# Performance work log

Hardware: AMD Instinct MI355X
Metric: run time of the kernel (lower is better)

The kernel has to match this reference:

```python
import jax, jax.numpy as jnp
import numpy as np

B, S, H, DK, DM = 8, 2048, 8, 64, 512  # batch, seq, heads, head dim, model dim
NEG = jnp.float32(-2**31)  # fill value for float32 per source


def setup_inputs() -> dict:
    key = jax.random.key(0)
    ks = jax.random.split(key, 8)
    q = jax.random.normal(ks[0], (B, S, DK), dtype=jnp.float32)
    k = jax.random.normal(ks[1], (B, S, DK), dtype=jnp.float32)
    v = jax.random.normal(ks[2], (B, S, DK), dtype=jnp.float32)
    mask = jax.random.randint(ks[3], (B, S, S), 0, 2).astype(jnp.float32)
    # torch Linear params stored as [in, out] for x @ W + b
    Wq = jax.random.normal(ks[4], (DK, H * DK), dtype=jnp.float32) / np.sqrt(DK).astype(np.float32)
    bq = jax.random.normal(ks[5], (H * DK,), dtype=jnp.float32) * 0.02
    Wo = jax.random.normal(ks[6], (H * DK, DM), dtype=jnp.float32) / np.sqrt(H * DK).astype(np.float32)
    bo = jax.random.normal(ks[7], (DM,), dtype=jnp.float32) * 0.02
    return {"q": q, "k": k, "v": v, "mask": mask, "Wq": Wq, "bq": bq, "Wo": Wo, "bo": bo}


def reference(q, k, v, mask, Wq, bq, Wo, bo):
    # Faithful to the source BUG: linear_q projects q, k AND v.
    def proj(x):
        b, s, _ = x.shape
        return (x @ Wq + bq).reshape(b, s, H, DK).transpose(2, 0, 1, 3)  # [H,B,S,DK]

    qh, kh, vh = proj(q), proj(k), proj(v)
    e = jnp.einsum('hbqd,hbkd->hbqk', qh, kh) / np.float32(np.sqrt(DK))  # [H,B,Sq,Sk]
    # source fills where ((mask-1).bool()==False), i.e. where mask == 1.0
    e = jnp.where(mask[None] == 1.0, NEG, e)
    a = jax.nn.softmax(e, axis=-1)
    y = jnp.einsum('hbqk,hbkd->hbqd', a, vh)          # [H,B,Sq,DK]
    y = y.transpose(1, 2, 0, 3).reshape(B, S, H * DK)  # [B,Sq,H*DK]
    return y @ Wo + bo
```

## Files before the change

kernel.cpp:

```cpp
#include <hip/hip_runtime.h>
#include <hip/hip_bf16.h>

#define BB 8
#define SS 2048
#define HD 512
#define DM 512

typedef __attribute__((ext_vector_type(8))) short short8;
typedef __attribute__((ext_vector_type(4))) short short4v;
typedef __attribute__((ext_vector_type(4))) float floatx4;

__device__ __forceinline__ short f2bf(float f) {
    __hip_bfloat16 h = __float2bfloat16(f);
    short s;
    __builtin_memcpy(&s, &h, 2);
    return s;
}

__device__ __forceinline__ uint2 pack4bf(float a, float b, float cc, float d) {
    __hip_bfloat162 lo = __float22bfloat162_rn(float2{a, b});
    __hip_bfloat162 hi = __float22bfloat162_rn(float2{cc, d});
    uint2 r;
    __builtin_memcpy(&r.x, &lo, 4);
    __builtin_memcpy(&r.y, &hi, 4);
    return r;
}

__device__ __forceinline__ short4v pack4bf_s4(float a, float b, float cc, float d) {
    uint2 u = pack4bf(a, b, cc, d);
    short4v s;
    __builtin_memcpy(&s, &u, 8);
    return s;
}

__device__ __forceinline__ floatx4 mfma16(short4v a, short4v b, floatx4 c) {
#if __has_builtin(__builtin_amdgcn_mfma_f32_16x16x16_bf16)
    return __builtin_amdgcn_mfma_f32_16x16x16_bf16(a, b, c, 0, 0, 0);
#else
    return __builtin_amdgcn_mfma_f32_16x16x16bf16_1k(a, b, c, 0, 0, 0);
#endif
}

__global__ void prep_kernel(const float* __restrict__ Wq, const float* __restrict__ Wo,
                            short* __restrict__ WqT, short* __restrict__ WoT) {
    int idx = blockIdx.x * 256 + threadIdx.x;
    if (idx < HD * 64) {
        int o = idx >> 6, i = idx & 63;
        WqT[idx] = f2bf(Wq[i * HD + o]);
    }
    {
        int o = idx >> 9, i = idx & 511;
        WoT[idx] = f2bf(Wo[i * DM + o]);
    }
}

__global__ void maskbits_kernel(const float* __restrict__ mask,
                                unsigned long long* __restrict__ bits) {
    int gw = blockIdx.x * 4 + (threadIdx.x >> 6);
    int lane = threadIdx.x & 63;
    size_t base = (size_t)gw * 256;
    float4 v = *(const float4*)(mask + base + (size_t)lane * 4);
    unsigned long long nib =
        (v.x == 1.0f ? 1ull : 0ull) | (v.y == 1.0f ? 2ull : 0ull) |
        (v.z == 1.0f ? 4ull : 0ull) | (v.w == 1.0f ? 8ull : 0ull);
    unsigned long long word = nib << (4 * (lane & 15));
    word |= __shfl_xor(word, 1);
    word |= __shfl_xor(word, 2);
    word |= __shfl_xor(word, 4);
    word |= __shfl_xor(word, 8);
    if ((lane & 15) == 0) bits[gw * 4 + (lane >> 4)] = word;
}

template <int SMODE, bool BIAS_ROW, bool A_F32, bool B_F32>
__global__ __launch_bounds__(256, 2) void gemm_bt(
    const void* __restrict__ A_, int lda, long sA,
    const void* __restrict__ B_, int ldb, long sB,
    void* __restrict__ C, int ldc, long sC,
    const float* __restrict__ bias, int K, float alpha) {
    const int bz = blockIdx.z;
    const int m0 = blockIdx.y * 128, n0 = blockIdx.x * 128;
    __shared__ __align__(16) short As[128 * 80];
    __shared__ __align__(16) short Bs[128 * 80];
    const int tid = threadIdx.x, lane = tid & 63, w = tid >> 6;
    const int c = lane & 15, Q = lane >> 4;
    const int wm = w >> 1, wn = w & 1;
    floatx4 acc[4][4] = {};

    for (int k0 = 0; k0 < K; k0 += 64) {
#pragma unroll
        for (int it = 0; it < 4; ++it) {
            int chunk = it * 256 + tid;
            int row = chunk >> 3, c8 = chunk & 7;
            size_t aoff = (size_t)bz * sA + (size_t)(m0 + row) * lda + k0 + c8 * 8;
            size_t boff = (size_t)bz * sB + (size_t)(n0 + row) * ldb + k0 + c8 * 8;
            if (A_F32) {
                const float* Af = (const float*)A_ + aoff;
                float4 lo = *(const float4*)Af;
                float4 hi = *(const float4*)(Af + 4);
                uint2 p0 = pack4bf(lo.x, lo.y, lo.z, lo.w);
                uint2 p1 = pack4bf(hi.x, hi.y, hi.z, hi.w);
                *(uint4*)&As[row * 80 + c8 * 8] = uint4{p0.x, p0.y, p1.x, p1.y};
            } else {
                *(uint4*)&As[row * 80 + c8 * 8] = *(const uint4*)((const short*)A_ + aoff);
            }
            if (B_F32) {
                const float* Bf = (const float*)B_ + boff;
                float4 lo = *(const float4*)Bf;
                float4 hi = *(const float4*)(Bf + 4);
                uint2 p0 = pack4bf(lo.x, lo.y, lo.z, lo.w);
                uint2 p1 = pack4bf(hi.x, hi.y, hi.z, hi.w);
                *(uint4*)&Bs[row * 80 + c8 * 8] = uint4{p0.x, p0.y, p1.x, p1.y};
            } else {
                *(uint4*)&Bs[row * 80 + c8 * 8] = *(const uint4*)((const short*)B_ + boff);
            }
        }
        __syncthreads();
#pragma unroll
        for (int ks = 0; ks < 2; ++ks) {
            short8 af[4], bf[4];
#pragma unroll
            for (int mt = 0; mt < 4; ++mt)
                af[mt] = *(const short8*)&As[(wm * 64 + mt * 16 + c) * 80 + ks * 32 + 8 * Q];
#pragma unroll
            for (int nt = 0; nt < 4; ++nt)
                bf[nt] = *(const short8*)&Bs[(wn * 64 + nt * 16 + c) * 80 + ks * 32 + 8 * Q];
#pragma unroll
            for (int mt = 0; mt < 4; ++mt)
#pragma unroll
                for (int nt = 0; nt < 4; ++nt)
                    acc[mt][nt] = __builtin_amdgcn_mfma_f32_16x16x32_bf16(
                        af[mt], bf[nt], acc[mt][nt], 0, 0, 0);
        }
        __syncthreads();
    }
#pragma unroll
    for (int mt = 0; mt < 4; ++mt)
#pragma unroll
        for (int nt = 0; nt < 4; ++nt) {
            int col = n0 + wn * 64 + nt * 16 + c;
            float bc = BIAS_ROW ? 0.f : bias[col];
#pragma unroll
            for (int r = 0; r < 4; ++r) {
                int row = m0 + wm * 64 + mt * 16 + 4 * Q + r;
                float val = (acc[mt][nt][r] + (BIAS_ROW ? bias[row] : bc)) * alpha;
                if (SMODE == 0) {
                    ((float*)C)[(size_t)bz * sC + (size_t)row * ldc + col] = val;
                } else if (SMODE == 1) {
                    ((short*)C)[(size_t)bz * sC + (size_t)row * ldc + col] = f2bf(val);
                } else if (SMODE == 2) {
                    int b = row >> 11, s = row & 2047, h = col >> 6, d = col & 63;
                    size_t idx = ((size_t)(b * 8 + h)) * 131072 + (size_t)s * 64 +
                                 (size_t)(((d >> 3) ^ (s & 7)) * 8 + (d & 7));
                    ((short*)C)[idx] = f2bf(val);
                } else {
                    int h = row >> 6, d = row & 63, s = col;
                    size_t idx = ((size_t)(bz * 8 + h)) * 131072 + (size_t)(s >> 3) * 512 +
                                 (size_t)((d ^ ((s >> 3) & 15)) * 8 + (s & 7));
                    ((short*)C)[idx] = f2bf(val);
                }
            }
        }
}

__global__ __launch_bounds__(512, 2) void fa_kernel(
    const short* __restrict__ qh, const short* __restrict__ khS,
    const short* __restrict__ vI, const unsigned* __restrict__ mbits,
    short* __restrict__ y) {
    const int id = blockIdx.x;
    const int xcd = id & 7, slot = id >> 3;
    const int qt = slot & 7;
    const int bh = (slot >> 3) * 8 + xcd;
    const int b = bh >> 3, h = bh & 7;
    const int tid = threadIdx.x, lane = tid & 63, w = tid >> 6;
    const int c = lane & 15, Q = lane >> 4;
    const int c7 = c & 7;

    __shared__ __align__(16) short Ks[8192];
    __shared__ __align__(16) short Vs[8192];

    const int qbase0 = qt * 256 + w * 32;
    short8 qf[2][2];
#pragma unroll
    for (int t = 0; t < 2; ++t) {
        const short* qb = qh + ((size_t)(b * SS + qbase0 + t * 16 + c)) * HD + h * 64;
        qf[t][0] = *(const short8*)(qb + 8 * Q);
        qf[t][1] = *(const short8*)(qb + 32 + 8 * Q);
    }
    const unsigned* mrow[2] = {
        mbits + (size_t)(b * SS + qbase0 + c) * 64,
        mbits + (size_t)(b * SS + qbase0 + 16 + c) * 64};

    const short* kbase = khS + (size_t)bh * 131072;
    const short* vbase = vI + (size_t)bh * 131072;

    floatx4 o[2][4] = {};
    float m_i[2] = {-INFINITY, -INFINITY}, l_i[2] = {0.f, 0.f};

    for (int kt = 0; kt < 16; ++kt) {
        const short* kg = kbase + kt * 8192;
        const short* vg = vbase + kt * 8192;
#pragma unroll
        for (int it = 0; it < 2; ++it) {
            int off = (it * 512 + tid) * 8;
            *(uint4*)&Ks[off] = *(const uint4*)(kg + off);
            *(uint4*)&Vs[off] = *(const uint4*)(vg + off);
        }
        uint4 mr[2];
#pragma unroll
        for (int t = 0; t < 2; ++t) mr[t] = *(const uint4*)(mrow[t] + kt * 4);
        __syncthreads();

        floatx4 s[2][8];
        float mx[2] = {-INFINITY, -INFINITY};
#pragma unroll
        for (int jt = 0; jt < 8; ++jt) {
            short8 k0 = *(const short8*)&Ks[(16 * jt + c) * 64 + ((Q) ^ c7) * 8];
            short8 k1 = *(const short8*)&Ks[(16 * jt + c) * 64 + ((Q + 4) ^ c7) * 8];
#pragma unroll
            for (int t = 0; t < 2; ++t) {
                floatx4 z = {};
                z = __builtin_amdgcn_mfma_f32_16x16x32_bf16(k0, qf[t][0], z, 0, 0, 0);
                z = __builtin_amdgcn_mfma_f32_16x16x32_bf16(k1, qf[t][1], z, 0, 0, 0);
                unsigned mwd = (jt & 2) ? ((jt & 4) ? mr[t].w : mr[t].y)
                                        : ((jt & 4) ? mr[t].z : mr[t].x);
                unsigned nib = (mwd >> (((jt & 1) << 4) + 4 * Q)) & 0xFu;
#pragma unroll
                for (int r = 0; r < 4; ++r) {
                    float val = (nib & (1u << r)) ? -INFINITY : z[r];
                    z[r] = val;
                    mx[t] = fmaxf(mx[t], val);
                }
                s[t][jt] = z;
            }
        }

        float al[2], msafe[2];
#pragma unroll
        for (int t = 0; t < 2; ++t) {
            float m = mx[t];
            m = fmaxf(m, __shfl_xor(m, 16));
            m = fmaxf(m, __shfl_xor(m, 32));
            float mnew = fmaxf(m_i[t], m);
            msafe[t] = (mnew == -INFINITY) ? 0.f : mnew;
            al[t] = __builtin_amdgcn_exp2f(m_i[t] - msafe[t]);
            m_i[t] = mnew;
#pragma unroll
            for (int r = 0; r < 4; ++r) {
                float alr = __shfl(al[t], 4 * Q + r);
#pragma unroll
                for (int nt = 0; nt < 4; ++nt) o[t][nt][r] *= alr;
            }
        }

        float ps[2] = {0.f, 0.f};
#pragma unroll
        for (int jt = 0; jt < 8; ++jt) {
            short4v af[2];
#pragma unroll
            for (int t = 0; t < 2; ++t) {
                float p0 = __builtin_amdgcn_exp2f(s[t][jt][0] - msafe[t]);
                float p1 = __builtin_amdgcn_exp2f(s[t][jt][1] - msafe[t]);
                float p2 = __builtin_amdgcn_exp2f(s[t][jt][2] - msafe[t]);
                float p3 = __builtin_amdgcn_exp2f(s[t][jt][3] - msafe[t]);
                ps[t] += (p0 + p1) + (p2 + p3);
                af[t] = pack4bf_s4(p0, p1, p2, p3);
            }
            const int g = 2 * jt + (Q >> 1);
            const int i4 = 4 * (Q & 1);
#pragma unroll
            for (int nt = 0; nt < 4; ++nt) {
                short4v vf = *(const short4v*)&Vs[g * 512 + ((16 * nt + c) ^ g) * 8 + i4];
                o[0][nt] = mfma16(af[0], vf, o[0][nt]);
                o[1][nt] = mfma16(af[1], vf, o[1][nt]);
            }
        }
#pragma unroll
        for (int t = 0; t < 2; ++t) {
            float p = ps[t];
            p += __shfl_xor(p, 16);
            p += __shfl_xor(p, 32);
            l_i[t] = l_i[t] * al[t] + p;
        }
        __syncthreads();
    }

#pragma unroll
    for (int t = 0; t < 2; ++t) {
#pragma unroll
        for (int r = 0; r < 4; ++r) {
            float lr = __shfl(l_i[t], 4 * Q + r);
            float inv = 1.0f / lr;
            int row = qbase0 + t * 16 + 4 * Q + r;
#pragma unroll
            for (int nt = 0; nt < 4; ++nt)
                y[((size_t)(b * SS + row)) * HD + h * 64 + 16 * nt + c] =
                    f2bf(o[t][nt][r] * inv);
        }
    }
}

extern "C" void kernel_launch(void* const* d_in, const int* in_sizes, int n_in,
                              void* d_out, int out_size, void* d_ws, size_t ws_size,
                              hipStream_t stream) {
    const float* q    = (const float*)d_in[0];
    const float* k    = (const float*)d_in[1];
    const float* v    = (const float*)d_in[2];
    const float* mask = (const float*)d_in[3];
    const float* Wq   = (const float*)d_in[4];
    const float* bq   = (const float*)d_in[5];
    const float* Wo   = (const float*)d_in[6];
    const float* bo   = (const float*)d_in[7];

    char* ws = (char*)d_ws;
    const size_t MB = 1ull << 20;
    short* WqT = (short*)(ws + 0 * MB);
    short* WoT = (short*)(ws + 1 * MB);
    short* qh  = (short*)(ws + 8 * MB);
    short* khS = (short*)(ws + 24 * MB);
    short* vI  = (short*)(ws + 40 * MB);
    unsigned long long* bits = (unsigned long long*)(ws + 56 * MB);
    short* yb  = (short*)(ws + 60 * MB);
    float* out = (float*)d_out;

    const float ALPHA_Q = 0.18033688011f;

    prep_kernel<<<1024, 256, 0, stream>>>(Wq, Wo, WqT, WoT);
    maskbits_kernel<<<32768, 256, 0, stream>>>(mask, bits);

    gemm_bt<1, false, true, false><<<dim3(4, 128, 1), 256, 0, stream>>>(
        q, 64, 0, WqT, 64, 0, (void*)qh, 512, 0, bq, 64, ALPHA_Q);
    gemm_bt<2, false, true, false><<<dim3(4, 128, 1), 256, 0, stream>>>(
        k, 64, 0, WqT, 64, 0, (void*)khS, 0, 0, bq, 64, 1.0f);
    gemm_bt<3, true, false, true><<<dim3(16, 4, BB), 256, 0, stream>>>(
        WqT, 64, 0, v, 64, (long)SS * 64, (void*)vI, 0, 0, bq, 64, 1.0f);

    fa_kernel<<<dim3(512, 1, 1), 512, 0, stream>>>(qh, khS, vI, (const unsigned*)bits, yb);

    gemm_bt<0, false, false, false><<<dim3(4, 128, 1), 256, 0, stream>>>(
        yb, 512, 0, WoT, 512, 0, (void*)out, 512, 0, bo, 512, 1.0f);
}
```

Before: 405.5 us.

## Double-buffer K/V tiles with async global-to-LDS loads and lazy softmax rescale

Doubles the K and V shared-memory buffers and prefetches the next tile with global_load_lds async copies while the current tile is computed, so tile loads overlap the MFMA work. This removes one barrier per iteration. It also adds a lazy rescale: the running max and output rescale are updated only when some lane's new max exceeds the old one by more than 8, otherwise alpha stays 1. The mask select is unrolled into a tree of fmax calls. Doubling LDS to 64KB may limit the two-blocks-per-CU occupancy. The sync placement for the async copies (no explicit vmcnt wait) may be fragile.

```diff
diff --git a/kernel.cpp b/kernel.cpp
--- a/kernel.cpp
+++ b/kernel.cpp
@@ -39,6 +39,12 @@
 #else
     return __builtin_amdgcn_mfma_f32_16x16x16bf16_1k(a, b, c, 0, 0, 0);
 #endif
+}
+
+__device__ __forceinline__ void async_copy16(const short* g, short* l) {
+    __builtin_amdgcn_global_load_lds(
+        (const __attribute__((address_space(1))) void*)g,
+        (__attribute__((address_space(3))) void*)l, 16, 0, 0);
 }
 
 __global__ void prep_kernel(const float* __restrict__ Wq, const float* __restrict__ Wo,
@@ -175,8 +181,18 @@
     const int c = lane & 15, Q = lane >> 4;
     const int c7 = c & 7;
 
-    __shared__ __align__(16) short Ks[8192];
-    __shared__ __align__(16) short Vs[8192];
+    __shared__ __align__(16) short Ks[2 * 8192];
+    __shared__ __align__(16) short Vs[2 * 8192];
+
+    const short* kbase = khS + (size_t)bh * 131072;
+    const short* vbase = vI + (size_t)bh * 131072;
+
+#pragma unroll
+    for (int it = 0; it < 2; ++it) {
+        int off = (it * 512 + tid) * 8;
+        async_copy16(kbase + off, &Ks[off]);
+        async_copy16(vbase + off, &Vs[off]);
+    }
 
     const int qbase0 = qt * 256 + w * 32;
     short8 qf[2][2];
@@ -190,32 +206,34 @@
         mbits + (size_t)(b * SS + qbase0 + c) * 64,
         mbits + (size_t)(b * SS + qbase0 + 16 + c) * 64};
 
-    const short* kbase = khS + (size_t)bh * 131072;
-    const short* vbase = vI + (size_t)bh * 131072;
-
     floatx4 o[2][4] = {};
     float m_i[2] = {-INFINITY, -INFINITY}, l_i[2] = {0.f, 0.f};
 
+    __syncthreads();
+
     for (int kt = 0; kt < 16; ++kt) {
-        const short* kg = kbase + kt * 8192;
-        const short* vg = vbase + kt * 8192;
-#pragma unroll
-        for (int it = 0; it < 2; ++it) {
-            int off = (it * 512 + tid) * 8;
-            *(uint4*)&Ks[off] = *(const uint4*)(kg + off);
-            *(uint4*)&Vs[off] = *(const uint4*)(vg + off);
+        const int cb = (kt & 1) * 8192;
+        if (kt < 15) {
+            const int nb = ((kt + 1) & 1) * 8192;
+            const short* kg = kbase + (kt + 1) * 8192;
+            const short* vg = vbase + (kt + 1) * 8192;
+#pragma unroll
+            for (int it = 0; it < 2; ++it) {
+                int off = (it * 512 + tid) * 8;
+                async_copy16(kg + off, &Ks[nb + off]);
+                async_copy16(vg + off, &Vs[nb + off]);
+            }
         }
         uint4 mr[2];
 #pragma unroll
         for (int t = 0; t < 2; ++t) mr[t] = *(const uint4*)(mrow[t] + kt * 4);
-        __syncthreads();
 
         floatx4 s[2][8];
         float mx[2] = {-INFINITY, -INFINITY};
 #pragma unroll
         for (int jt = 0; jt < 8; ++jt) {
-            short8 k0 = *(const short8*)&Ks[(16 * jt + c) * 64 + ((Q) ^ c7) * 8];
-            short8 k1 = *(const short8*)&Ks[(16 * jt + c) * 64 + ((Q + 4) ^ c7) * 8];
+            short8 k0 = *(const short8*)&Ks[cb + (16 * jt + c) * 64 + ((Q) ^ c7) * 8];
+            short8 k1 = *(const short8*)&Ks[cb + (16 * jt + c) * 64 + ((Q + 4) ^ c7) * 8];
 #pragma unroll
             for (int t = 0; t < 2; ++t) {
                 floatx4 z = {};
@@ -224,12 +242,12 @@
                 unsigned mwd = (jt & 2) ? ((jt & 4) ? mr[t].w : mr[t].y)
                                         : ((jt & 4) ? mr[t].z : mr[t].x);
                 unsigned nib = (mwd >> (((jt & 1) << 4) + 4 * Q)) & 0xFu;
-#pragma unroll
-                for (int r = 0; r < 4; ++r) {
-                    float val = (nib & (1u << r)) ? -INFINITY : z[r];
-                    z[r] = val;
-                    mx[t] = fmaxf(mx[t], val);
-                }
+                float v0 = (nib & 1u) ? -INFINITY : z[0];
+                float v1 = (nib & 2u) ? -INFINITY : z[1];
+                float v2 = (nib & 4u) ? -INFINITY : z[2];
+                float v3 = (nib & 8u) ? -INFINITY : z[3];
+                z[0] = v0; z[1] = v1; z[2] = v2; z[3] = v3;
+                mx[t] = fmaxf(mx[t], fmaxf(fmaxf(v0, v1), fmaxf(v2, v3)));
                 s[t][jt] = z;
             }
         }
@@ -240,15 +258,20 @@
             float m = mx[t];
             m = fmaxf(m, __shfl_xor(m, 16));
             m = fmaxf(m, __shfl_xor(m, 32));
-            float mnew = fmaxf(m_i[t], m);
-            msafe[t] = (mnew == -INFINITY) ? 0.f : mnew;
-            al[t] = __builtin_amdgcn_exp2f(m_i[t] - msafe[t]);
-            m_i[t] = mnew;
-#pragma unroll
-            for (int r = 0; r < 4; ++r) {
-                float alr = __shfl(al[t], 4 * Q + r);
-#pragma unroll
-                for (int nt = 0; nt < 4; ++nt) o[t][nt][r] *= alr;
+            if (__all(m - m_i[t] <= 8.0f)) {
+                al[t] = 1.0f;
+                msafe[t] = (m_i[t] == -INFINITY) ? 0.f : m_i[t];
+            } else {
+                float mnew = fmaxf(m_i[t], m);
+                msafe[t] = (mnew == -INFINITY) ? 0.f : mnew;
+                al[t] = __builtin_amdgcn_exp2f(m_i[t] - msafe[t]);
+                m_i[t] = mnew;
+#pragma unroll
+                for (int r = 0; r < 4; ++r) {
+                    float alr = __shfl(al[t], 4 * Q + r);
+#pragma unroll
+                    for (int nt = 0; nt < 4; ++nt) o[t][nt][r] *= alr;
+                }
             }
         }
 
@@ -269,7 +292,7 @@
             const int i4 = 4 * (Q & 1);
 #pragma unroll
             for (int nt = 0; nt < 4; ++nt) {
-                short4v vf = *(const short4v*)&Vs[g * 512 + ((16 * nt + c) ^ g) * 8 + i4];
+                short4v vf = *(const short4v*)&Vs[cb + g * 512 + ((16 * nt + c) ^ g) * 8 + i4];
                 o[0][nt] = mfma16(af[0], vf, o[0][nt]);
                 o[1][nt] = mfma16(af[1], vf, o[1][nt]);
             }
@@ -281,7 +304,7 @@
             p += __shfl_xor(p, 32);
             l_i[t] = l_i[t] * al[t] + p;
         }
-        __syncthreads();
+        if (kt < 15) __syncthreads();
     }
 
 #pragma unroll
```

Measured after the change: 398.6 us. About the same (-1.7%).

## Restructure flash attention with async double-buffered LDS loads and lazy rescaling

Applied to the files above, without the earlier changes.

Reworks the attention kernel to use one 16-row query tile per wave, 1024 blocks with launch bounds allowing 8 blocks per CU, and 64-key tiles double-buffered in LDS through global_load_lds async copies so the next tile loads while the current one computes. Softmax is fused into a single score pass that uses the running max and only rescales and recomputes when the max grows by more than a threshold. The V layout written by the projection GEMM changes so PV can use 16x16x32 MFMAs with 8-element loads. The cost is possible recomputation of scores on max jumps, more syncs per key, and reliance on the async LDS copy ordering.

```diff
diff --git a/kernel.cpp b/kernel.cpp
--- a/kernel.cpp
+++ b/kernel.cpp
@@ -33,12 +33,10 @@
     return s;
 }
 
-__device__ __forceinline__ floatx4 mfma16(short4v a, short4v b, floatx4 c) {
-#if __has_builtin(__builtin_amdgcn_mfma_f32_16x16x16_bf16)
-    return __builtin_amdgcn_mfma_f32_16x16x16_bf16(a, b, c, 0, 0, 0);
-#else
-    return __builtin_amdgcn_mfma_f32_16x16x16bf16_1k(a, b, c, 0, 0, 0);
-#endif
+__device__ __forceinline__ void async_copy16(const short* g, short* l) {
+    __builtin_amdgcn_global_load_lds(
+        (const __attribute__((address_space(1))) void*)g,
+        (__attribute__((address_space(3))) void*)l, 16, 0, 0);
 }
 
 __global__ void prep_kernel(const float* __restrict__ Wq, const float* __restrict__ Wo,
@@ -154,148 +152,144 @@
                     ((short*)C)[idx] = f2bf(val);
                 } else {
                     int h = row >> 6, d = row & 63, s = col;
-                    size_t idx = ((size_t)(bz * 8 + h)) * 131072 + (size_t)(s >> 3) * 512 +
-                                 (size_t)((d ^ ((s >> 3) & 15)) * 8 + (s & 7));
+                    int J = s >> 5;
+                    int j = 4 * ((s >> 4) & 1) + (s & 3);
+                    int Qm = (s >> 2) & 3;
+                    int slotm = Qm ^ ((d >> 1) & 3);
+                    size_t idx = ((size_t)(bz * 8 + h)) * 131072 + (size_t)J * 2048 +
+                                 (size_t)(d * 32 + slotm * 8 + j);
                     ((short*)C)[idx] = f2bf(val);
                 }
             }
         }
 }
 
-__global__ __launch_bounds__(512, 2) void fa_kernel(
+__global__ __launch_bounds__(512, 8) void fa_kernel(
     const short* __restrict__ qh, const short* __restrict__ khS,
     const short* __restrict__ vI, const unsigned* __restrict__ mbits,
     short* __restrict__ y) {
     const int id = blockIdx.x;
     const int xcd = id & 7, slot = id >> 3;
-    const int qt = slot & 7;
-    const int bh = (slot >> 3) * 8 + xcd;
+    const int qt = slot & 15;
+    const int bh = (slot >> 4) * 8 + xcd;
     const int b = bh >> 3, h = bh & 7;
     const int tid = threadIdx.x, lane = tid & 63, w = tid >> 6;
     const int c = lane & 15, Q = lane >> 4;
     const int c7 = c & 7;
-
-    __shared__ __align__(16) short Ks[8192];
-    __shared__ __align__(16) short Vs[8192];
-
-    const int qbase0 = qt * 256 + w * 32;
-    short8 qf[2][2];
-#pragma unroll
-    for (int t = 0; t < 2; ++t) {
-        const short* qb = qh + ((size_t)(b * SS + qbase0 + t * 16 + c)) * HD + h * 64;
-        qf[t][0] = *(const short8*)(qb + 8 * Q);
-        qf[t][1] = *(const short8*)(qb + 32 + 8 * Q);
-    }
-    const unsigned* mrow[2] = {
-        mbits + (size_t)(b * SS + qbase0 + c) * 64,
-        mbits + (size_t)(b * SS + qbase0 + 16 + c) * 64};
+    const int vslot = Q ^ ((c >> 1) & 3);
+
+    __shared__ __align__(16) short Ks[2 * 4096];
+    __shared__ __align__(16) short Vs[2 * 4096];
 
     const short* kbase = khS + (size_t)bh * 131072;
     const short* vbase = vI + (size_t)bh * 131072;
-
-    floatx4 o[2][4] = {};
-    float m_i[2] = {-INFINITY, -INFINITY}, l_i[2] = {0.f, 0.f};
-
-    for (int kt = 0; kt < 16; ++kt) {
-        const short* kg = kbase + kt * 8192;
-        const short* vg = vbase + kt * 8192;
-#pragma unroll
-        for (int it = 0; it < 2; ++it) {
-            int off = (it * 512 + tid) * 8;
-            *(uint4*)&Ks[off] = *(const uint4*)(kg + off);
-            *(uint4*)&Vs[off] = *(const uint4*)(vg + off);
+    const int soff = tid * 8;
+
+    async_copy16(kbase + soff, &Ks[soff]);
+    async_copy16(vbase + soff, &Vs[soff]);
+
+    const int qbase0 = qt * 128 + w * 16;
+    const short* qb = qh + ((size_t)(b * SS + qbase0 + c)) * HD + h * 64;
+    short8 qf0 = *(const short8*)(qb + 8 * Q);
+    short8 qf1 = *(const short8*)(qb + 32 + 8 * Q);
+    const unsigned* mrow = mbits + (size_t)(b * SS + qbase0 + c) * 64;
+
+    floatx4 o[4] = {};
+    float m_i = -INFINITY, l_i = 0.f;
+
+    __syncthreads();
+
+    for (int kt2 = 0; kt2 < 16; ++kt2) {
+        uint4 mr4 = *(const uint4*)(mrow + kt2 * 4);
+#pragma unroll
+        for (int hf = 0; hf < 2; ++hf) {
+            const int kt = 2 * kt2 + hf;
+            const int cb = hf * 4096;
+            const int nb = (1 - hf) * 4096;
+            const unsigned mlo = hf ? mr4.z : mr4.x;
+            const unsigned mhi = hf ? mr4.w : mr4.y;
+
+            if (kt < 31) {
+                const short* kg = kbase + (kt + 1) * 4096;
+                const short* vg = vbase + (kt + 1) * 4096;
+                async_copy16(kg + soff, &Ks[nb + soff]);
+                async_copy16(vg + soff, &Vs[nb + soff]);
+            }
+
+            float mx = -INFINITY;
+            short4v p4[4];
+            auto score_pass = [&](float msafe_) -> float {
+                float ps_ = 0.f;
+#pragma unroll
+                for (int jt = 0; jt < 4; ++jt) {
+                    short8 k0 = *(const short8*)&Ks[cb + (16 * jt + c) * 64 + (Q ^ c7) * 8];
+                    short8 k1 = *(const short8*)&Ks[cb + (16 * jt + c) * 64 + ((Q + 4) ^ c7) * 8];
+                    floatx4 z = {};
+                    z = __builtin_amdgcn_mfma_f32_16x16x32_bf16(k0, qf0, z, 0, 0, 0);
+                    z = __builtin_amdgcn_mfma_f32_16x16x32_bf16(k1, qf1, z, 0, 0, 0);
+                    unsigned mwd = (jt & 2) ? mhi : mlo;
+                    unsigned nib = (mwd >> (((jt & 1) << 4) + 4 * Q)) & 0xFu;
+                    float v0 = (nib & 1u) ? -INFINITY : z[0];
+                    float v1 = (nib & 2u) ? -INFINITY : z[1];
+                    float v2 = (nib & 4u) ? -INFINITY : z[2];
+                    float v3 = (nib & 8u) ? -INFINITY : z[3];
+                    mx = fmaxf(mx, fmaxf(fmaxf(v0, v1), fmaxf(v2, v3)));
+                    float p0 = __builtin_amdgcn_exp2f(v0 - msafe_);
+                    float p1 = __builtin_amdgcn_exp2f(v1 - msafe_);
+                    float p2 = __builtin_amdgcn_exp2f(v2 - msafe_);
+                    float p3 = __builtin_amdgcn_exp2f(v3 - msafe_);
+                    ps_ += (p0 + p1) + (p2 + p3);
+                    p4[jt] = pack4bf_s4(p0, p1, p2, p3);
+                }
+                return ps_;
+            };
+
+            float msafe0 = (m_i == -INFINITY) ? 0.f : m_i;
+            float ps = score_pass(msafe0);
+            mx = fmaxf(mx, __shfl_xor(mx, 16));
+            mx = fmaxf(mx, __shfl_xor(mx, 32));
+            if (!__all(mx - m_i <= 8.0f)) {
+                float mnew = fmaxf(m_i, mx);
+                float msafe1 = (mnew == -INFINITY) ? 0.f : mnew;
+                float al = __builtin_amdgcn_exp2f(m_i - msafe1);
+                m_i = mnew;
+#pragma unroll
+                for (int r = 0; r < 4; ++r) {
+                    float alr = __shfl(al, 4 * Q + r);
+#pragma unroll
+                    for (int nt = 0; nt < 4; ++nt) o[nt][r] *= alr;
+                }
+                l_i *= al;
+                ps = score_pass(msafe1);
+            }
+
+#pragma unroll
+            for (int J = 0; J < 2; ++J) {
+                union { short4v h[2]; short8 v8; } u;
+                u.h[0] = p4[2 * J];
+                u.h[1] = p4[2 * J + 1];
+#pragma unroll
+                for (int nt = 0; nt < 4; ++nt) {
+                    short8 vf = *(const short8*)&Vs[cb + J * 2048 + (16 * nt + c) * 32 + vslot * 8];
+                    o[nt] = __builtin_amdgcn_mfma_f32_16x16x32_bf16(u.v8, vf, o[nt], 0, 0, 0);
+                }
+            }
+            ps += __shfl_xor(ps, 16);
+            ps += __shfl_xor(ps, 32);
+            l_i += ps;
+            if (kt < 31) __syncthreads();
         }
-        uint4 mr[2];
-#pragma unroll
-        for (int t = 0; t < 2; ++t) mr[t] = *(const uint4*)(mrow[t] + kt * 4);
-        __syncthreads();
-
-        floatx4 s[2][8];
-        float mx[2] = {-INFINITY, -INFINITY};
-#pragma unroll
-        for (int jt = 0; jt < 8; ++jt) {
-            short8 k0 = *(const short8*)&Ks[(16 * jt + c) * 64 + ((Q) ^ c7) * 8];
-            short8 k1 = *(const short8*)&Ks[(16 * jt + c) * 64 + ((Q + 4) ^ c7) * 8];
-#pragma unroll
-            for (int t = 0; t < 2; ++t) {
-                floatx4 z = {};
-                z = __builtin_amdgcn_mfma_f32_16x16x32_bf16(k0, qf[t][0], z, 0, 0, 0);
-                z = __builtin_amdgcn_mfma_f32_16x16x32_bf16(k1, qf[t][1], z, 0, 0, 0);
-                unsigned mwd = (jt & 2) ? ((jt & 4) ? mr[t].w : mr[t].y)
-                                        : ((jt & 4) ? mr[t].z : mr[t].x);
-                unsigned nib = (mwd >> (((jt & 1) << 4) + 4 * Q)) & 0xFu;
-#pragma unroll
-                for (int r = 0; r < 4; ++r) {
-                    float val = (nib & (1u << r)) ? -INFINITY : z[r];
-                    z[r] = val;
-                    mx[t] = fmaxf(mx[t], val);
-                }
-                s[t][jt] = z;
-            }
-        }
-
-        float al[2], msafe[2];
-#pragma unroll
-        for (int t = 0; t < 2; ++t) {
-            float m = mx[t];
-            m = fmaxf(m, __shfl_xor(m, 16));
-            m = fmaxf(m, __shfl_xor(m, 32));
-            float mnew = fmaxf(m_i[t], m);
-            msafe[t] = (mnew == -INFINITY) ? 0.f : mnew;
-            al[t] = __builtin_amdgcn_exp2f(m_i[t] - msafe[t]);
-            m_i[t] = mnew;
-#pragma unroll
-            for (int r = 0; r < 4; ++r) {
-                float alr = __shfl(al[t], 4 * Q + r);
-#pragma unroll
-                for (int nt = 0; nt < 4; ++nt) o[t][nt][r] *= alr;
-            }
-        }
-
-        float ps[2] = {0.f, 0.f};
-#pragma unroll
-        for (int jt = 0; jt < 8; ++jt) {
-            short4v af[2];
-#pragma unroll
-            for (int t = 0; t < 2; ++t) {
-                float p0 = __builtin_amdgcn_exp2f(s[t][jt][0] - msafe[t]);
-                float p1 = __builtin_amdgcn_exp2f(s[t][jt][1] - msafe[t]);
-                float p2 = __builtin_amdgcn_exp2f(s[t][jt][2] - msafe[t]);
-                float p3 = __builtin_amdgcn_exp2f(s[t][jt][3] - msafe[t]);
-                ps[t] += (p0 + p1) + (p2 + p3);
-                af[t] = pack4bf_s4(p0, p1, p2, p3);
-            }
-            const int g = 2 * jt + (Q >> 1);
-            const int i4 = 4 * (Q & 1);
-#pragma unroll
-            for (int nt = 0; nt < 4; ++nt) {
-                short4v vf = *(const short4v*)&Vs[g * 512 + ((16 * nt + c) ^ g) * 8 + i4];
-                o[0][nt] = mfma16(af[0], vf, o[0][nt]);
-                o[1][nt] = mfma16(af[1], vf, o[1][nt]);
-            }
-        }
-#pragma unroll
-        for (int t = 0; t < 2; ++t) {
-            float p = ps[t];
-            p += __shfl_xor(p, 16);
-            p += __shfl_xor(p, 32);
-            l_i[t] = l_i[t] * al[t] + p;
-        }
-        __syncthreads();
-    }
-
-#pragma unroll
-    for (int t = 0; t < 2; ++t) {
-#pragma unroll
-        for (int r = 0; r < 4; ++r) {
-            float lr = __shfl(l_i[t], 4 * Q + r);
-            float inv = 1.0f / lr;
-            int row = qbase0 + t * 16 + 4 * Q + r;
-#pragma unroll
-            for (int nt = 0; nt < 4; ++nt)
-                y[((size_t)(b * SS + row)) * HD + h * 64 + 16 * nt + c] =
-                    f2bf(o[t][nt][r] * inv);
-        }
+    }
+
+#pragma unroll
+    for (int r = 0; r < 4; ++r) {
+        float lr = __shfl(l_i, 4 * Q + r);
+        float inv = 1.0f / lr;
+        int row = qbase0 + 4 * Q + r;
+#pragma unroll
+        for (int nt = 0; nt < 4; ++nt)
+            y[((size_t)(b * SS + row)) * HD + h * 64 + 16 * nt + c] =
+                f2bf(o[nt][r] * inv);
     }
 }
 
@@ -334,7 +328,7 @@
     gemm_bt<3, true, false, true><<<dim3(16, 4, BB), 256, 0, stream>>>(
         WqT, 64, 0, v, 64, (long)SS * 64, (void*)vI, 0, 0, bq, 64, 1.0f);
 
-    fa_kernel<<<dim3(512, 1, 1), 512, 0, stream>>>(qh, khS, vI, (const unsigned*)bits, yb);
+    fa_kernel<<<dim3(1024, 1, 1), 512, 0, stream>>>(qh, khS, vI, (const unsigned*)bits, yb);
 
     gemm_bt<0, false, false, false><<<dim3(4, 128, 1), 256, 0, stream>>>(
         yb, 512, 0, WoT, 512, 0, (void*)out, 512, 0, bo, 512, 1.0f);
```

New measurement: 960.1 us. 137% more time.
